# Performance work log

Measured on AMD Instinct MI355X. Metric: run time of the kernel, lower is better.

The kernel has to match this reference:

```python
import jax, jax.numpy as jnp
from jax import lax
import numpy as np

N_CLUSTERS = 512
MAX_ITER = 10
N_SAMPLES = 400000
N_FEATURES = 128


def setup_inputs() -> dict:
    key = jax.random.key(0)
    kx, ki = jax.random.split(key)
    X = jax.random.normal(kx, (N_SAMPLES, N_FEATURES), dtype=jnp.float32)
    # init centroids = K random (with-replacement) rows of X, mimicking kmeans seeding
    idx = jax.random.randint(ki, (N_CLUSTERS,), 0, N_SAMPLES)
    init_centroids = X[idx]
    return {"X": X, "init_centroids": init_centroids}


def reference(X, init_centroids):
    """Lloyd's k-means: MAX_ITER iterations of cdist -> argmin -> segment-mean.
    Returns (cluster_centers [K,D], labels [N] int32, inertia scalar)."""
    K = init_centroids.shape[0]
    n = X.shape[0]
    x_sq = jnp.sum(X * X, axis=1, keepdims=True)            # [N,1], loop-invariant
    ones = jnp.ones((n,), dtype=X.dtype)

    def step(cent, _):
        c_sq = jnp.sum(cent * cent, axis=1)                  # [K]
        # squared euclidean distances (cdist^2); argmin/min order matches cdist
        d2 = x_sq - 2.0 * (X @ cent.T) + c_sq[None, :]       # [N,K]
        labels = jnp.argmin(d2, axis=1)                      # [N]
        inertia = jnp.sum(jnp.maximum(jnp.min(d2, axis=1), 0.0))
        sums = jax.ops.segment_sum(X, labels, num_segments=K)          # [K,D]
        counts = jax.ops.segment_sum(ones, labels, num_segments=K)     # [K]
        means = sums / jnp.maximum(counts, 1.0)[:, None]
        # empty cluster -> keep old centroid (torch branch: (labels==k).sum()>0)
        new_cent = jnp.where(counts[:, None] > 0, means, cent)
        return new_cent, (labels, inertia)

    centroids, (labels_hist, inertia_hist) = lax.scan(
        step, init_centroids, None, length=MAX_ITER)
    return centroids, labels_hist[-1], inertia_hist[-1]
```

## Files before the change

kernel.cpp:

```cpp
#include <hip/hip_runtime.h>

#define N_S 400000
#define N_F 128
#define N_K 512
#define ITERS 10

typedef __attribute__((ext_vector_type(8))) short short8;
typedef __attribute__((ext_vector_type(4))) float floatx4;

__device__ inline unsigned short f2bf(float f) {
    unsigned int u = __float_as_uint(f);
    unsigned int r = (u + 0x7FFFu + ((u >> 16) & 1u)) >> 16;
    return (unsigned short)r;
}

__device__ inline unsigned int cvt_pk_bf16(float lo, float hi) {
    unsigned int r;
    asm("v_cvt_pk_bf16_f32 %0, %1, %2" : "=v"(r) : "v"(lo), "v"(hi));
    return r;
}

__device__ inline void gload_lds16(const void* g, void* l) {
    __builtin_amdgcn_global_load_lds(
        (const __attribute__((address_space(1))) void*)g,
        (__attribute__((address_space(3))) void*)l, 16, 0, 0);
}

__device__ inline void put_sw(unsigned short* __restrict__ swhi, int k, int d, float v) {
    int c = k >> 5, mm = k & 31;
    int mt = mm >> 4, m = mm & 15;
    int kt = d >> 5, r = d & 31;
    int quad = r >> 3, j = r & 7;
    int lane = quad * 16 + m;
    int idx = ((c * 8 + mt * 4 + kt) * 64 + lane) * 8 + j;
    swhi[idx] = f2bf(v);
}

__global__ __launch_bounds__(64) void prep_update_kernel(
    const float* __restrict__ src, float* __restrict__ cent,
    float* __restrict__ sums, int* __restrict__ ihist,
    float* __restrict__ c_sq, unsigned short* __restrict__ swhi,
    int* __restrict__ cursor, float* __restrict__ inertia, int do_update) {
    int k = blockIdx.x, lane = threadIdx.x;
    float a, b;
    float cnt = (float)ihist[k];
    if (do_update) {
        float sa = sums[k * N_F + lane], sb = sums[k * N_F + 64 + lane];
        float olda = cent[k * N_F + lane], oldb = cent[k * N_F + 64 + lane];
        a = (cnt > 0.f) ? (sa / cnt) : olda;
        b = (cnt > 0.f) ? (sb / cnt) : oldb;
    } else {
        a = src[k * N_F + lane];
        b = src[k * N_F + 64 + lane];
    }
    cent[k * N_F + lane] = a;
    cent[k * N_F + 64 + lane] = b;
    sums[k * N_F + lane] = 0.f;
    sums[k * N_F + 64 + lane] = 0.f;
    put_sw(swhi, k, lane, a);
    put_sw(swhi, k, lane + 64, b);
    float s = fmaf(a, a, b * b);
#pragma unroll
    for (int off = 32; off > 0; off >>= 1) s += __shfl_down(s, off);
    if (lane == 0) {
        c_sq[k] = s;
        ihist[k] = 0;
        cursor[k] = 0;
        if (k == 0) *inertia = 0.f;
    }
}

#define CHUNK 32
#define NTN 4

__global__ __launch_bounds__(256, 2) void assign_kernel(
    const float* __restrict__ X,
    const unsigned short* __restrict__ swhi,
    const float* __restrict__ c_sq,
    float* __restrict__ labels,
    float* __restrict__ inertia,
    int* __restrict__ ihist) {
    __shared__ __align__(16) short8 a_lds[2][2 * 8 * 64];
    __shared__ __align__(16) float csq_s[N_K];
    __shared__ int lhist[N_K];
    __shared__ float red[4];

    int t = threadIdx.x;
    int w = t >> 6, l = t & 63;
    int quad = l >> 4, l15 = l & 15;
    long long S0 = (long long)blockIdx.x * 256;

    {
        const char* gq = (const char*)swhi + t * 16;
        char* lq = (char*)a_lds[0] + t * 16;
#pragma unroll
        for (int i = 0; i < 4; ++i) gload_lds16(gq + i * 4096, lq + i * 4096);
    }

    for (int i = t; i < N_K; i += 256) {
        lhist[i] = 0;
        csq_s[i] = c_sq[i];
    }

    short8 bhi[NTN][4];
    float xsqv[NTN];
    long long srow[NTN];
#pragma unroll
    for (int nt = 0; nt < NTN; ++nt) {
        long long s = S0 + w * 64 + nt * 16 + l15;
        srow[nt] = s;
        long long ss = (s < N_S) ? s : (N_S - 1);
        const float4* xp = (const float4*)(X + ss * N_F);
        float sq = 0.f;
#pragma unroll
        for (int kt = 0; kt < 4; ++kt) {
            float4 va = xp[kt * 8 + quad * 2];
            float4 vb = xp[kt * 8 + quad * 2 + 1];
            float f[8] = {va.x, va.y, va.z, va.w, vb.x, vb.y, vb.z, vb.w};
            short8 h;
            unsigned int* hw = (unsigned int*)&h;
            hw[0] = cvt_pk_bf16(f[0], f[1]);
            hw[1] = cvt_pk_bf16(f[2], f[3]);
            hw[2] = cvt_pk_bf16(f[4], f[5]);
            hw[3] = cvt_pk_bf16(f[6], f[7]);
#pragma unroll
            for (int j = 0; j < 8; ++j) sq = fmaf(f[j], f[j], sq);
            bhi[nt][kt] = h;
        }
        sq += __shfl_xor(sq, 16);
        sq += __shfl_xor(sq, 32);
        xsqv[nt] = sq;
    }

    __syncthreads();

    float best[NTN];
    int bestk[NTN];
#pragma unroll
    for (int nt = 0; nt < NTN; ++nt) { best[nt] = 3.4e38f; bestk[nt] = 0; }

#pragma unroll
    for (int p = 0; p < 8; ++p) {
        if (p < 7) {
            const char* gq = (const char*)swhi + (p + 1) * 16384 + t * 16;
            char* lq = (char*)a_lds[(p + 1) & 1] + t * 16;
#pragma unroll
            for (int i = 0; i < 4; ++i) gload_lds16(gq + i * 4096, lq + i * 4096);
        }

        const short8* abase = a_lds[p & 1] + l;
#pragma unroll
        for (int cc = 0; cc < 2; ++cc) {
            int c = p * 2 + cc;
            floatx4 acc[2][NTN];
#pragma unroll
            for (int mt = 0; mt < 2; ++mt)
#pragma unroll
                for (int nt = 0; nt < NTN; ++nt) acc[mt][nt] = (floatx4){0.f, 0.f, 0.f, 0.f};

#pragma unroll
            for (int kt = 0; kt < 4; ++kt) {
                short8 a0 = abase[(cc * 8 + kt) * 64];
                short8 a1 = abase[(cc * 8 + 4 + kt) * 64];
#pragma unroll
                for (int nt = 0; nt < NTN; ++nt) {
                    acc[0][nt] = __builtin_amdgcn_mfma_f32_16x16x32_bf16(a0, bhi[nt][kt], acc[0][nt], 0, 0, 0);
                    acc[1][nt] = __builtin_amdgcn_mfma_f32_16x16x32_bf16(a1, bhi[nt][kt], acc[1][nt], 0, 0, 0);
                }
            }

#pragma unroll
            for (int mt = 0; mt < 2; ++mt) {
                float4 cs = ((const float4*)csq_s)[c * 8 + mt * 4 + quad];
#pragma unroll
                for (int r = 0; r < 4; ++r) {
                    float csr = (r == 0) ? cs.x : (r == 1) ? cs.y : (r == 2) ? cs.z : cs.w;
                    int kg = c * CHUNK + mt * 16 + quad * 4 + r;
#pragma unroll
                    for (int nt = 0; nt < NTN; ++nt) {
                        float d2 = fmaf(-2.f, acc[mt][nt][r], csr);
                        if (d2 < best[nt]) { best[nt] = d2; bestk[nt] = kg; }
                    }
                }
            }
        }

        if (p < 7) __syncthreads();
    }

#pragma unroll
    for (int nt = 0; nt < NTN; ++nt) {
#pragma unroll
        for (int off = 16; off < 64; off <<= 1) {
            float ob = __shfl_xor(best[nt], off);
            int ok = __shfl_xor(bestk[nt], off);
            if (ob < best[nt] || (ob == best[nt] && ok < bestk[nt])) {
                best[nt] = ob;
                bestk[nt] = ok;
            }
        }
    }

    float contrib = 0.f;
    if (quad == 0) {
#pragma unroll
        for (int nt = 0; nt < NTN; ++nt) {
            if (srow[nt] < N_S) {
                labels[srow[nt]] = (float)bestk[nt];
                atomicAdd(&lhist[bestk[nt]], 1);
                contrib += fmaxf(xsqv[nt] + best[nt], 0.f);
            }
        }
    }
#pragma unroll
    for (int off = 32; off > 0; off >>= 1) contrib += __shfl_down(contrib, off);
    if (l == 0) red[w] = contrib;
    __syncthreads();
    if (t == 0) atomicAdd(inertia, red[0] + red[1] + red[2] + red[3]);

    for (int i = t; i < N_K; i += 256) {
        int v = lhist[i];
        if (v) atomicAdd(&ihist[i], v);
    }
}

__global__ __launch_bounds__(256) void scatter_kernel(const float* __restrict__ labels,
                                                      const int* __restrict__ ihist,
                                                      int* __restrict__ cursor,
                                                      int* __restrict__ order) {
    __shared__ int lhist[N_K];
    __shared__ int excl[N_K];
    __shared__ int lbase[N_K];
    __shared__ int wtot[4];
    int t = threadIdx.x;
    long long i0 = (long long)blockIdx.x * 1024 + (long long)t * 4;

    for (int j = t; j < N_K; j += 256) lhist[j] = 0;

    int v0 = ihist[2 * t], v1 = ihist[2 * t + 1];
    int s = v0 + v1;
    int x = s;
    int lane = t & 63, w = t >> 6;
#pragma unroll
    for (int off = 1; off < 64; off <<= 1) {
        int y = __shfl_up(x, off);
        if (lane >= off) x += y;
    }
    if (lane == 63) wtot[w] = x;
    __syncthreads();
    int woff = 0;
    for (int ww = 0; ww < w; ++ww) woff += wtot[ww];
    int ex = woff + x - s;
    excl[2 * t] = ex;
    excl[2 * t + 1] = ex + v0;

    int k0 = 0, k1 = 0, k2 = 0, k3 = 0, r0 = 0, r1 = 0, r2 = 0, r3 = 0;
    bool valid = (i0 < N_S);
    if (valid) {
        float4 lab = *(const float4*)(labels + i0);
        k0 = (int)lab.x; k1 = (int)lab.y; k2 = (int)lab.z; k3 = (int)lab.w;
        r0 = atomicAdd(&lhist[k0], 1);
        r1 = atomicAdd(&lhist[k1], 1);
        r2 = atomicAdd(&lhist[k2], 1);
        r3 = atomicAdd(&lhist[k3], 1);
    }
    __syncthreads();
    for (int j = t; j < N_K; j += 256) {
        int c = lhist[j];
        lbase[j] = c ? (excl[j] + atomicAdd(&cursor[j], c)) : 0;
    }
    __syncthreads();
    if (valid) {
        int i = (int)i0;
        order[lbase[k0] + r0] = ((i + 0) << 9) | k0;
        order[lbase[k1] + r1] = ((i + 1) << 9) | k1;
        order[lbase[k2] + r2] = ((i + 2) << 9) | k2;
        order[lbase[k3] + r3] = ((i + 3) << 9) | k3;
    }
}

#define RPB 256

__device__ inline void flush4(float* __restrict__ sums, int k, int dbase, float4 acc) {
    float* sp = sums + k * N_F + dbase;
    atomicAdd(sp + 0, acc.x);
    atomicAdd(sp + 1, acc.y);
    atomicAdd(sp + 2, acc.z);
    atomicAdd(sp + 3, acc.w);
}

__global__ __launch_bounds__(256) void csum_kernel(const float* __restrict__ X,
                                                   const int* __restrict__ order,
                                                   float* __restrict__ sums) {
    __shared__ int ord_s[RPB];
    __shared__ float part[8][N_F];
    int t = threadIdx.x;
    int r0 = blockIdx.x * RPB;
    int nvalid = min(RPB, N_S - r0);
    if (t < nvalid) ord_s[t] = order[r0 + t];
    __syncthreads();

    int g = t >> 5;
    int dbase = (t & 31) << 2;
    const float* Xd = X + dbase;
    int base = g * 32;
    int gend = min(base + 32, nvalid);

    int kfirst = ord_s[0] & 511;
    int klast = ord_s[nvalid - 1] & 511;

    if (kfirst == klast) {
        float4 acc = {0.f, 0.f, 0.f, 0.f};
#pragma unroll 8
        for (int i = base; i < gend; ++i) {
            int row = ord_s[i] >> 9;
            const float4 v = *(const float4*)(Xd + (long long)row * N_F);
            acc.x += v.x; acc.y += v.y; acc.z += v.z; acc.w += v.w;
        }
        *(float4*)&part[g][dbase] = acc;
        __syncthreads();
        if (t < N_F) {
            float r = 0.f;
#pragma unroll
            for (int gg = 0; gg < 8; ++gg) r += part[gg][t];
            atomicAdd(&sums[kfirst * N_F + t], r);
        }
    } else {
        float4 acc = {0.f, 0.f, 0.f, 0.f};
        int kcur = (base < gend) ? (ord_s[base] & 511) : -1;
        for (int i = base; i < gend; ++i) {
            int e = ord_s[i];
            int k = e & 511;
            if (k != kcur) {
                flush4(sums, kcur, dbase, acc);
                acc = (float4){0.f, 0.f, 0.f, 0.f};
                kcur = k;
            }
            const float4 v = *(const float4*)(Xd + (long long)(e >> 9) * N_F);
            acc.x += v.x; acc.y += v.y; acc.z += v.z; acc.w += v.w;
        }
        if (kcur >= 0) flush4(sums, kcur, dbase, acc);
    }
}

__global__ __launch_bounds__(128) void update_kernel(const float* __restrict__ sums,
                                                     const int* __restrict__ ihist,
                                                     float* __restrict__ cent) {
    int k = blockIdx.x;
    int d = threadIdx.x;
    float c = (float)ihist[k];
    float s = sums[k * N_F + d];
    float old = cent[k * N_F + d];
    cent[k * N_F + d] = (c > 0.f) ? (s / c) : old;
}

extern "C" void kernel_launch(void* const* d_in, const int* in_sizes, int n_in,
                              void* d_out, int out_size, void* d_ws, size_t ws_size,
                              hipStream_t stream) {
    const float* X = (const float*)d_in[0];
    const float* initc = (const float*)d_in[1];

    float* out = (float*)d_out;
    float* cent = out;
    float* labels = out + N_K * N_F;
    float* inertia = labels + N_S;

    float* c_sq = (float*)d_ws;
    float* sums = c_sq + N_K;
    unsigned short* swhi = (unsigned short*)(sums + N_K * N_F);
    int* ihist = (int*)(swhi + N_K * N_F);
    int* cursor = ihist + N_K;
    int* order = cursor + N_K;

    for (int it = 0; it < ITERS; ++it) {
        prep_update_kernel<<<N_K, 64, 0, stream>>>(initc, cent, sums, ihist, c_sq,
                                                   swhi, cursor, inertia, it > 0);
        assign_kernel<<<(N_S + 255) / 256, 256, 0, stream>>>(X, swhi, c_sq,
                                                             labels, inertia, ihist);
        scatter_kernel<<<(N_S + 1023) / 1024, 256, 0, stream>>>(labels, ihist, cursor,
                                                                order);
        csum_kernel<<<(N_S + RPB - 1) / RPB, 256, 0, stream>>>(X, order, sums);
    }
    update_kernel<<<N_K, N_F, 0, stream>>>(sums, ihist, cent);
}
```

Measured before the change: 1.784 ms.

## Make assign kernel persistent with full centroid matrix resident in LDS

The assign kernel becomes a persistent grid of 256 blocks with 512 threads. Each block loads the whole bf16 centroid matrix (128 KB) into LDS once, then loops over 512-sample tiles, where it previously streamed centroid chunks with double buffering and a barrier per chunk. This removes the repeated centroid reloads and the per-chunk barriers, and it also reduces the LDS histogram and inertia flush to one per block. MFMA sections get raised wave priority through s_setprio. In exchange, occupancy drops to one block per CU, and the X loads are no longer overlapped with another block's compute except through the 8 waves within the block.

```diff
diff --git a/kernel.cpp b/kernel.cpp
--- a/kernel.cpp
+++ b/kernel.cpp
@@ -72,102 +72,101 @@
 
 #define CHUNK 32
 #define NTN 4
-
-__global__ __launch_bounds__(256, 2) void assign_kernel(
+#define TILE 512
+#define NTILES ((N_S + TILE - 1) / TILE)
+#define AGRID 256
+
+__global__ __launch_bounds__(512, 1) void assign_kernel(
     const float* __restrict__ X,
     const unsigned short* __restrict__ swhi,
     const float* __restrict__ c_sq,
     float* __restrict__ labels,
     float* __restrict__ inertia,
     int* __restrict__ ihist) {
-    __shared__ __align__(16) short8 a_lds[2][2 * 8 * 64];
+    __shared__ __align__(16) short8 a_lds[16 * 8 * 64];
     __shared__ __align__(16) float csq_s[N_K];
     __shared__ int lhist[N_K];
-    __shared__ float red[4];
+    __shared__ float red[8];
 
     int t = threadIdx.x;
     int w = t >> 6, l = t & 63;
     int quad = l >> 4, l15 = l & 15;
-    long long S0 = (long long)blockIdx.x * 256;
 
     {
         const char* gq = (const char*)swhi + t * 16;
-        char* lq = (char*)a_lds[0] + t * 16;
-#pragma unroll
-        for (int i = 0; i < 4; ++i) gload_lds16(gq + i * 4096, lq + i * 4096);
-    }
-
-    for (int i = t; i < N_K; i += 256) {
+        char* lq = (char*)a_lds + t * 16;
+#pragma unroll
+        for (int i = 0; i < 16; ++i) gload_lds16(gq + i * 8192, lq + i * 8192);
+    }
+
+    for (int i = t; i < N_K; i += 512) {
         lhist[i] = 0;
         csq_s[i] = c_sq[i];
     }
 
-    short8 bhi[NTN][4];
-    float xsqv[NTN];
-    long long srow[NTN];
-#pragma unroll
-    for (int nt = 0; nt < NTN; ++nt) {
-        long long s = S0 + w * 64 + nt * 16 + l15;
-        srow[nt] = s;
-        long long ss = (s < N_S) ? s : (N_S - 1);
-        const float4* xp = (const float4*)(X + ss * N_F);
-        float sq = 0.f;
-#pragma unroll
-        for (int kt = 0; kt < 4; ++kt) {
-            float4 va = xp[kt * 8 + quad * 2];
-            float4 vb = xp[kt * 8 + quad * 2 + 1];
-            float f[8] = {va.x, va.y, va.z, va.w, vb.x, vb.y, vb.z, vb.w};
-            short8 h;
-            unsigned int* hw = (unsigned int*)&h;
-            hw[0] = cvt_pk_bf16(f[0], f[1]);
-            hw[1] = cvt_pk_bf16(f[2], f[3]);
-            hw[2] = cvt_pk_bf16(f[4], f[5]);
-            hw[3] = cvt_pk_bf16(f[6], f[7]);
-#pragma unroll
-            for (int j = 0; j < 8; ++j) sq = fmaf(f[j], f[j], sq);
-            bhi[nt][kt] = h;
-        }
-        sq += __shfl_xor(sq, 16);
-        sq += __shfl_xor(sq, 32);
-        xsqv[nt] = sq;
-    }
-
-    __syncthreads();
-
-    float best[NTN];
-    int bestk[NTN];
-#pragma unroll
-    for (int nt = 0; nt < NTN; ++nt) { best[nt] = 3.4e38f; bestk[nt] = 0; }
-
-#pragma unroll
-    for (int p = 0; p < 8; ++p) {
-        if (p < 7) {
-            const char* gq = (const char*)swhi + (p + 1) * 16384 + t * 16;
-            char* lq = (char*)a_lds[(p + 1) & 1] + t * 16;
-#pragma unroll
-            for (int i = 0; i < 4; ++i) gload_lds16(gq + i * 4096, lq + i * 4096);
-        }
-
-        const short8* abase = a_lds[p & 1] + l;
-#pragma unroll
-        for (int cc = 0; cc < 2; ++cc) {
-            int c = p * 2 + cc;
+    __syncthreads();
+
+    const short8* abase = a_lds + l;
+    float inert = 0.f;
+
+    for (int tile = blockIdx.x; tile < NTILES; tile += AGRID) {
+        long long S0 = (long long)tile * TILE + w * 64;
+
+        short8 bhi[NTN][4];
+        float xsqv[NTN];
+        long long srow[NTN];
+#pragma unroll
+        for (int nt = 0; nt < NTN; ++nt) {
+            long long s = S0 + nt * 16 + l15;
+            srow[nt] = s;
+            long long ss = (s < N_S) ? s : (N_S - 1);
+            const float4* xp = (const float4*)(X + ss * N_F);
+            float sq = 0.f;
+#pragma unroll
+            for (int kt = 0; kt < 4; ++kt) {
+                float4 va = xp[kt * 8 + quad * 2];
+                float4 vb = xp[kt * 8 + quad * 2 + 1];
+                float f[8] = {va.x, va.y, va.z, va.w, vb.x, vb.y, vb.z, vb.w};
+                short8 h;
+                unsigned int* hw = (unsigned int*)&h;
+                hw[0] = cvt_pk_bf16(f[0], f[1]);
+                hw[1] = cvt_pk_bf16(f[2], f[3]);
+                hw[2] = cvt_pk_bf16(f[4], f[5]);
+                hw[3] = cvt_pk_bf16(f[6], f[7]);
+#pragma unroll
+                for (int j = 0; j < 8; ++j) sq = fmaf(f[j], f[j], sq);
+                bhi[nt][kt] = h;
+            }
+            sq += __shfl_xor(sq, 16);
+            sq += __shfl_xor(sq, 32);
+            xsqv[nt] = sq;
+        }
+
+        float best[NTN];
+        int bestk[NTN];
+#pragma unroll
+        for (int nt = 0; nt < NTN; ++nt) { best[nt] = 3.4e38f; bestk[nt] = 0; }
+
+#pragma unroll 4
+        for (int c = 0; c < 16; ++c) {
             floatx4 acc[2][NTN];
 #pragma unroll
             for (int mt = 0; mt < 2; ++mt)
 #pragma unroll
                 for (int nt = 0; nt < NTN; ++nt) acc[mt][nt] = (floatx4){0.f, 0.f, 0.f, 0.f};
 
+            __builtin_amdgcn_s_setprio(1);
 #pragma unroll
             for (int kt = 0; kt < 4; ++kt) {
-                short8 a0 = abase[(cc * 8 + kt) * 64];
-                short8 a1 = abase[(cc * 8 + 4 + kt) * 64];
+                short8 a0 = abase[(c * 8 + kt) * 64];
+                short8 a1 = abase[(c * 8 + 4 + kt) * 64];
 #pragma unroll
                 for (int nt = 0; nt < NTN; ++nt) {
                     acc[0][nt] = __builtin_amdgcn_mfma_f32_16x16x32_bf16(a0, bhi[nt][kt], acc[0][nt], 0, 0, 0);
                     acc[1][nt] = __builtin_amdgcn_mfma_f32_16x16x32_bf16(a1, bhi[nt][kt], acc[1][nt], 0, 0, 0);
                 }
             }
+            __builtin_amdgcn_s_setprio(0);
 
 #pragma unroll
             for (int mt = 0; mt < 2; ++mt) {
@@ -185,40 +184,42 @@
             }
         }
 
-        if (p < 7) __syncthreads();
-    }
-
-#pragma unroll
-    for (int nt = 0; nt < NTN; ++nt) {
-#pragma unroll
-        for (int off = 16; off < 64; off <<= 1) {
-            float ob = __shfl_xor(best[nt], off);
-            int ok = __shfl_xor(bestk[nt], off);
-            if (ob < best[nt] || (ob == best[nt] && ok < bestk[nt])) {
-                best[nt] = ob;
-                bestk[nt] = ok;
-            }
-        }
-    }
-
-    float contrib = 0.f;
-    if (quad == 0) {
 #pragma unroll
         for (int nt = 0; nt < NTN; ++nt) {
-            if (srow[nt] < N_S) {
-                labels[srow[nt]] = (float)bestk[nt];
-                atomicAdd(&lhist[bestk[nt]], 1);
-                contrib += fmaxf(xsqv[nt] + best[nt], 0.f);
-            }
-        }
-    }
-#pragma unroll
-    for (int off = 32; off > 0; off >>= 1) contrib += __shfl_down(contrib, off);
-    if (l == 0) red[w] = contrib;
-    __syncthreads();
-    if (t == 0) atomicAdd(inertia, red[0] + red[1] + red[2] + red[3]);
-
-    for (int i = t; i < N_K; i += 256) {
+#pragma unroll
+            for (int off = 16; off < 64; off <<= 1) {
+                float ob = __shfl_xor(best[nt], off);
+                int ok = __shfl_xor(bestk[nt], off);
+                if (ob < best[nt] || (ob == best[nt] && ok < bestk[nt])) {
+                    best[nt] = ob;
+                    bestk[nt] = ok;
+                }
+            }
+        }
+
+        if (quad == 0) {
+#pragma unroll
+            for (int nt = 0; nt < NTN; ++nt) {
+                if (srow[nt] < N_S) {
+                    labels[srow[nt]] = (float)bestk[nt];
+                    atomicAdd(&lhist[bestk[nt]], 1);
+                    inert += fmaxf(xsqv[nt] + best[nt], 0.f);
+                }
+            }
+        }
+    }
+
+#pragma unroll
+    for (int off = 32; off > 0; off >>= 1) inert += __shfl_down(inert, off);
+    if (l == 0) red[w] = inert;
+    __syncthreads();
+    if (t == 0) {
+        float s = 0.f;
+#pragma unroll
+        for (int i = 0; i < 8; ++i) s += red[i];
+        atomicAdd(inertia, s);
+    }
+    for (int i = t; i < N_K; i += 512) {
         int v = lhist[i];
         if (v) atomicAdd(&ihist[i], v);
     }
@@ -375,8 +376,8 @@
     for (int it = 0; it < ITERS; ++it) {
         prep_update_kernel<<<N_K, 64, 0, stream>>>(initc, cent, sums, ihist, c_sq,
                                                    swhi, cursor, inertia, it > 0);
-        assign_kernel<<<(N_S + 255) / 256, 256, 0, stream>>>(X, swhi, c_sq,
-                                                             labels, inertia, ihist);
+        assign_kernel<<<AGRID, 512, 0, stream>>>(X, swhi, c_sq,
+                                                 labels, inertia, ihist);
         scatter_kernel<<<(N_S + 1023) / 1024, 256, 0, stream>>>(labels, ihist, cursor,
                                                                 order);
         csum_kernel<<<(N_S + RPB - 1) / RPB, 256, 0, stream>>>(X, order, sums);
```

Measured after the change: 1.535 ms. 14.0% less time.
